# Performance work log

Hardware: AMD Instinct MI355X
Metric: run time of the kernel (lower is better)

The kernel has to match this reference:

```python
import jax, jax.numpy as jnp
import numpy as np

N_NODES = 100000
N_EDGES = 1200000
IN_CH = 64
HID = 16
OUT_CH = 64
EDGE_DIM = 3


def _glorot(key, shape):
    fan_in, fan_out = shape[0], shape[1]
    lim = float(np.sqrt(6.0 / (fan_in + fan_out)))
    return jax.random.uniform(key, shape, jnp.float32, -lim, lim)


def setup_inputs() -> dict:
    key = jax.random.key(0)
    ks = jax.random.split(key, 16)
    x = jax.random.normal(ks[0], (N_NODES, IN_CH), jnp.float32)
    edge_index = jax.random.randint(ks[1], (2, N_EDGES), 0, N_NODES, jnp.int64)
    edge_attr = jax.random.normal(ks[2], (N_EDGES, EDGE_DIM), jnp.float32)
    return {
        "x": x,
        "edge_index": edge_index,
        "edge_attr": edge_attr,
        # conv1: in->16
        "W1l": _glorot(ks[3], (IN_CH, HID)), "b1l": jnp.zeros((HID,), jnp.float32),
        "W1r": _glorot(ks[4], (IN_CH, HID)), "b1r": jnp.zeros((HID,), jnp.float32),
        "W1e": _glorot(ks[5], (EDGE_DIM, IN_CH)), "b1e": jnp.zeros((IN_CH,), jnp.float32),
        # conv2: 16->out
        "W2l": _glorot(ks[6], (HID, OUT_CH)), "b2l": jnp.zeros((OUT_CH,), jnp.float32),
        "W2r": _glorot(ks[7], (HID, OUT_CH)), "b2r": jnp.zeros((OUT_CH,), jnp.float32),
        "W2e": _glorot(ks[8], (EDGE_DIM, HID)), "b2e": jnp.zeros((HID,), jnp.float32),
    }


def _sage_conv(x, src, dst, edge_attr, We, be, Wl, bl, Wr, br):
    # message: neighbor feature + projected edge attribute (edge_dim-aware SAGE)
    msg = x[src] + edge_attr @ We + be                       # [E, C_in]
    agg = jax.ops.segment_sum(msg, dst, num_segments=N_NODES)  # [N, C_in]
    deg = jax.ops.segment_sum(jnp.ones((msg.shape[0],), msg.dtype), dst,
                              num_segments=N_NODES)
    agg = agg / jnp.maximum(deg, 1.0)[:, None]               # mean aggregation
    return agg @ Wl + bl + x @ Wr + br                       # neighbor + self paths


def reference(x, edge_index, edge_attr,
              W1l, b1l, W1r, b1r, W1e, b1e,
              W2l, b2l, W2r, b2r, W2e, b2e):
    src, dst = edge_index[0], edge_index[1]
    h = jax.nn.relu(_sage_conv(x, src, dst, edge_attr, W1e, b1e, W1l, b1l, W1r, b1r))
    # F.dropout(training=self.training): eval mode -> identity
    out = _sage_conv(h, src, dst, edge_attr, W2e, b2e, W2l, b2l, W2r, b2r)
    return out
```

## Files before the change

kernel.cpp:

```cpp
#include <hip/hip_runtime.h>
#include <hip/hip_bf16.h>
#include <stdint.h>

#define N_NODES 100000
#define N_EDGES 1200000
#define IN_CH 64
#define HID 16
#define OUT_CH 64

#define BN 100
#define NB 1000
#define BCAP 2048
#define CAP 2048

#define F_TPB 512
#define KY_BLOCKS ((N_NODES * 2 + F_TPB - 1) / F_TPB)
#define SC_EPB 2048
#define SC_EPT (SC_EPB / F_TPB)
#define SC_BLOCKS ((N_EDGES + SC_EPB - 1) / SC_EPB)
#define F_GROUPS 196

typedef __hip_bfloat16 bf16;

__device__ __forceinline__ float b2f(bf16 v) { return __bfloat162float(v); }
__device__ __forceinline__ float lo_f(uint32_t p) { return __uint_as_float(p << 16); }
__device__ __forceinline__ float hi_f(uint32_t p) { return __uint_as_float(p & 0xffff0000u); }
__device__ __forceinline__ uint16_t f2bb(float v) {
    bf16 h = __float2bfloat16(v);
    return *reinterpret_cast<uint16_t*>(&h);
}

__device__ __forceinline__ float loadf(const void* p, size_t i, int bf) {
    return bf ? b2f(((const bf16*)p)[i]) : ((const float*)p)[i];
}
__device__ __forceinline__ uint32_t bfbits(const void* p, size_t i, int bf) {
    if (bf) return ((const uint16_t*)p)[i];
    return f2bb(((const float*)p)[i]);
}
__device__ __forceinline__ int ld_dst(const int* p, int j, int i64) {
    if (i64) return ((const int2*)p)[(size_t)N_EDGES + j].x;
    return p[(size_t)N_EDGES + j];
}
__device__ __forceinline__ int ld_src(const int* p, int j, int i64) {
    if (i64) return ((const int2*)p)[j].x;
    return p[j];
}

__device__ __forceinline__ int detect_bf(const void* x) {
    const uint16_t* u = (const uint16_t*)x;
    int cnt = 0;
    for (int i = 0; i < 64; ++i) {
        int e = (u[i] >> 7) & 0xff;
        cnt += (e >= 100 && e <= 140);
    }
    return cnt >= 50;
}
__device__ __forceinline__ int detect_i64(const int* ei) {
    const uint32_t* w = (const uint32_t*)ei;
    int z = 0;
    for (int i = 1; i < 64; i += 2) z += (w[i] == 0u);
    return z >= 16;
}

__global__ void __launch_bounds__(F_TPB) k_fused(const void* __restrict__ x,
                                                 const int* __restrict__ ei,
                                                 const void* __restrict__ ea,
                                                 const void* __restrict__ W1l,
                                                 const void* __restrict__ W1r,
                                                 const void* __restrict__ b1l,
                                                 const void* __restrict__ b1r,
                                                 const void* __restrict__ W1e,
                                                 const void* __restrict__ b1e,
                                                 bf16* __restrict__ y,
                                                 bf16* __restrict__ zh,
                                                 float* __restrict__ wc,
                                                 int* __restrict__ gcnt,
                                                 uint2* __restrict__ slots,
                                                 uint16_t* __restrict__ ea2v) {
    __shared__ __align__(16) char smem[36608];
    __shared__ int wsum[8];
    __shared__ int s_flags;
    int t = threadIdx.x;
    int g = blockIdx.x / 5, r = blockIdx.x % 5;
    if (t == 0) s_flags = detect_bf(x) | (detect_i64(ei) << 1);

    if (r < 2) {
        int kyid = g * 2 + r;
        if (kyid >= KY_BLOCKS) return;
        float* w = (float*)smem;
        float* bz = (float*)(smem + 8192);
        __syncthreads();
        int bf = s_flags & 1;
        for (int i = t; i < IN_CH * 32; i += F_TPB) {
            int k = i >> 5, cc = i & 31;
            w[i] = (cc < 16) ? loadf(W1l, k * HID + cc, bf)
                             : loadf(W1r, k * HID + (cc - 16), bf);
        }
        if (t < HID) bz[t] = loadf(b1l, t, bf) + loadf(b1r, t, bf);
        __syncthreads();
        if (kyid == 0 && t < HID) {
            int j = t;
            float s0 = 0.f, s1 = 0.f, s2 = 0.f, s3 = 0.f;
            for (int k = 0; k < IN_CH; ++k) {
                float wl = w[k * 32 + j];
                s0 += loadf(W1e, k, bf) * wl;
                s1 += loadf(W1e, IN_CH + k, bf) * wl;
                s2 += loadf(W1e, 2 * IN_CH + k, bf) * wl;
                s3 += loadf(b1e, k, bf) * wl;
            }
            wc[j] = s0;
            wc[HID + j] = s1;
            wc[2 * HID + j] = s2;
            wc[3 * HID + j] = s3;
        }
        int tid = kyid * F_TPB + t;
        int row = tid >> 1;
        if (row >= N_NODES) return;
        int half = tid & 1, cs = half * 16;
        float acc[16];
#pragma unroll
        for (int j = 0; j < 16; ++j) acc[j] = 0.f;
        if (bf) {
            const uint4* xr = (const uint4*)((const uint16_t*)x + (size_t)row * IN_CH);
            uint4 q[8];
#pragma unroll
            for (int i = 0; i < 8; ++i) q[i] = xr[i];
            const uint32_t* qq = (const uint32_t*)q;
#pragma unroll
            for (int k2 = 0; k2 < 32; ++k2) {
                uint32_t u = qq[k2];
                float x0 = lo_f(u), x1 = hi_f(u);
                const float* w0 = &w[(2 * k2) * 32 + cs];
                const float* w1 = w0 + 32;
#pragma unroll
                for (int j = 0; j < 16; ++j) acc[j] += x0 * w0[j] + x1 * w1[j];
            }
        } else {
            const float4* xr = (const float4*)((const float*)x + (size_t)row * IN_CH);
#pragma unroll
            for (int c = 0; c < 4; ++c) {
                float4 f[4];
#pragma unroll
                for (int i = 0; i < 4; ++i) f[i] = xr[c * 4 + i];
                const float* ff = (const float*)f;
#pragma unroll
                for (int kk = 0; kk < 16; ++kk) {
                    float xk = ff[kk];
                    const float* wr = &w[(c * 16 + kk) * 32 + cs];
#pragma unroll
                    for (int j = 0; j < 16; ++j) acc[j] += xk * wr[j];
                }
            }
        }
        if (half) {
#pragma unroll
            for (int j = 0; j < 16; ++j) acc[j] += bz[j];
        }
        uint32_t pk[8];
#pragma unroll
        for (int j2 = 0; j2 < 8; ++j2)
            pk[j2] = (uint32_t)f2bb(acc[2 * j2]) | ((uint32_t)f2bb(acc[2 * j2 + 1]) << 16);
        bf16* dst = half ? (zh + (size_t)row * HID) : (y + (size_t)row * HID);
        uint4* d4 = (uint4*)dst;
        d4[0] = make_uint4(pk[0], pk[1], pk[2], pk[3]);
        d4[1] = make_uint4(pk[4], pk[5], pk[6], pk[7]);
        return;
    }

    int scid = g * 3 + (r - 2);
    if (scid >= SC_BLOCKS) return;
    uint2* lval = (uint2*)smem;
    int* lhist = (int*)(smem + 16384);
    int* lscan = (int*)(smem + 20384);
    int* ldelta = (int*)(smem + 24384);
    uint16_t* lea = (uint16_t*)(smem + 28384);
    uint16_t* lbid = (uint16_t*)(smem + 32480);
    for (int i = t; i < NB; i += F_TPB) lhist[i] = 0;
    __syncthreads();
    int bf = s_flags & 1, i64 = (s_flags >> 1) & 1;
    int base = scid * SC_EPB;
    uint32_t rb[SC_EPT], srcv[SC_EPT], ea01v[SC_EPT], ea2r[SC_EPT];
#pragma unroll
    for (int i = 0; i < SC_EPT; ++i) {
        int e = base + i * F_TPB + t;
        rb[i] = 0xFFFFFFFFu;
        if (e < N_EDGES) {
            uint32_t d = (uint32_t)ld_dst(ei, e, i64);
            srcv[i] = (uint32_t)ld_src(ei, e, i64);
            ea01v[i] = bfbits(ea, (size_t)e * 3, bf) |
                       (bfbits(ea, (size_t)e * 3 + 1, bf) << 16);
            ea2r[i] = bfbits(ea, (size_t)e * 3 + 2, bf);
            uint32_t b = d / BN;
            uint32_t dl = d - b * BN;
            uint32_t rr = (uint32_t)atomicAdd(&lhist[b], 1);
            rb[i] = (b << 19) | (dl << 12) | rr;
        }
    }
    __syncthreads();
    int b0 = 2 * t, b1 = 2 * t + 1;
    int cnt0 = (b0 < NB) ? lhist[b0] : 0;
    int cnt1 = (b1 < NB) ? lhist[b1] : 0;
    int s_local = cnt0 + cnt1;
    int incl = s_local;
    int lane = t & 63;
#pragma unroll
    for (int d = 1; d < 64; d <<= 1) {
        int v = __shfl_up(incl, d);
        if (lane >= d) incl += v;
    }
    int w = t >> 6;
    if (lane == 63) wsum[w] = incl;
    __syncthreads();
    int wbase = 0, nst = 0;
#pragma unroll
    for (int i = 0; i < 8; ++i) {
        int v = wsum[i];
        wbase += (i < w) ? v : 0;
        nst += v;
    }
    int run = wbase + incl - s_local;
    if (b0 < NB) {
        lscan[b0] = run;
        if (cnt0) ldelta[b0] = b0 * BCAP + atomicAdd(&gcnt[b0], cnt0) - run;
    }
    run += cnt0;
    if (b1 < NB) {
        lscan[b1] = run;
        if (cnt1) ldelta[b1] = b1 * BCAP + atomicAdd(&gcnt[b1], cnt1) - run;
    }
    __syncthreads();
#pragma unroll
    for (int i = 0; i < SC_EPT; ++i) {
        if (rb[i] == 0xFFFFFFFFu) continue;
        uint32_t b = rb[i] >> 19;
        uint32_t dl = (rb[i] >> 12) & 0x7Fu;
        uint32_t rr = rb[i] & 0xFFFu;
        int lp = lscan[b] + (int)rr;
        lval[lp] = make_uint2(srcv[i] | (dl << 17), ea01v[i]);
        lea[lp] = (uint16_t)ea2r[i];
        lbid[lp] = (uint16_t)b;
    }
    __syncthreads();
    for (int p = t; p < nst; p += F_TPB) {
        int b = lbid[p];
        int gp = ldelta[b] + p;
        slots[gp] = lval[p];
        ea2v[gp] = lea[p];
    }
}

__global__ void __launch_bounds__(256) k_agg1(const uint2* __restrict__ slots,
                                              const uint16_t* __restrict__ ea2v,
                                              const int* __restrict__ gcnt,
                                              const bf16* __restrict__ y,
                                              const float* __restrict__ wc,
                                              bf16* __restrict__ zh,
                                              float* __restrict__ sa,
                                              uint32_t* __restrict__ ssrc,
                                              int* __restrict__ nof2) {
    __shared__ uint2 su[CAP];
    __shared__ uint16_t ea2s[CAP];
    __shared__ uint32_t sst[CAP];
    __shared__ uint32_t sea01[CAP];
    __shared__ uint16_t sea2[CAP];
    __shared__ int hist[BN], noff[BN], cur[BN];
    __shared__ int wsum[4];
    __shared__ float swc[64];
    int t = threadIdx.x;
    if (t < 64) swc[t] = wc[t];
    int b = blockIdx.x;
    int n = gcnt[b];
    if (n > CAP) n = CAP;
    const uint2* sp = slots + (size_t)b * BCAP;
    const uint16_t* ep = ea2v + (size_t)b * BCAP;
    int dl = t >> 1, half = t & 1, cs = half * 8;

    for (int i = t; i < BN; i += 256) hist[i] = 0;
    for (int i = t; i < n; i += 256) {
        su[i] = sp[i];
        ea2s[i] = ep[i];
    }
    __syncthreads();
    for (int i = t; i < n; i += 256) atomicAdd(&hist[su[i].x >> 17], 1);
    __syncthreads();
    {
        int own = (t < BN) ? hist[t] : 0;
        int incl = own;
        int lane = t & 63;
#pragma unroll
        for (int d = 1; d < 64; d <<= 1) {
            int v = __shfl_up(incl, d);
            if (lane >= d) incl += v;
        }
        int w = t >> 6;
        if (lane == 63) wsum[w] = incl;
        __syncthreads();
        int wbase = 0;
#pragma unroll
        for (int i = 0; i < 4; ++i) wbase += (i < w) ? wsum[i] : 0;
        if (t < BN) {
            int ex = wbase + incl - own;
            noff[t] = ex;
            cur[t] = ex;
        }
        __syncthreads();
    }
    for (int i = t; i < n; i += 256) {
        uint2 u2 = su[i];
        int r = atomicAdd(&cur[u2.x >> 17], 1);
        sst[r] = u2.x;
        sea01[r] = u2.y;
        sea2[r] = ea2s[i];
    }
    __syncthreads();
    for (int p = t; p < n; p += 256) ssrc[(size_t)b * BCAP + p] = sst[p];
    if (t < BN) nof2[b * 128 + t] = noff[t];
    float acc[16];
#pragma unroll
    for (int j = 0; j < 16; ++j) acc[j] = 0.f;
    float a0 = 0.f, a1 = 0.f, a2 = 0.f, degT = 0.f;
    if (dl < BN) {
        int kb = noff[dl];
        int ke = (dl == BN - 1) ? n : noff[dl + 1];
        degT = (float)(ke - kb);
        int k = kb + half;
        for (; k + 2 < ke; k += 4) {
            uint32_t s0 = sst[k], s1 = sst[k + 2];
            const uint32_t* r0 = (const uint32_t*)(y + (size_t)(s0 & 0x1FFFFu) * HID);
            const uint32_t* r1 = (const uint32_t*)(y + (size_t)(s1 & 0x1FFFFu) * HID);
            uint4 qa = *(const uint4*)r0;
            uint4 qb = *(const uint4*)(r0 + 4);
            uint4 qc = *(const uint4*)r1;
            uint4 qd = *(const uint4*)(r1 + 4);
            acc[0] += lo_f(qa.x) + lo_f(qc.x); acc[1] += hi_f(qa.x) + hi_f(qc.x);
            acc[2] += lo_f(qa.y) + lo_f(qc.y); acc[3] += hi_f(qa.y) + hi_f(qc.y);
            acc[4] += lo_f(qa.z) + lo_f(qc.z); acc[5] += hi_f(qa.z) + hi_f(qc.z);
            acc[6] += lo_f(qa.w) + lo_f(qc.w); acc[7] += hi_f(qa.w) + hi_f(qc.w);
            acc[8] += lo_f(qb.x) + lo_f(qd.x); acc[9] += hi_f(qb.x) + hi_f(qd.x);
            acc[10] += lo_f(qb.y) + lo_f(qd.y); acc[11] += hi_f(qb.y) + hi_f(qd.y);
            acc[12] += lo_f(qb.z) + lo_f(qd.z); acc[13] += hi_f(qb.z) + hi_f(qd.z);
            acc[14] += lo_f(qb.w) + lo_f(qd.w); acc[15] += hi_f(qb.w) + hi_f(qd.w);
            uint32_t e0 = sea01[k], e1 = sea01[k + 2];
            a0 += lo_f(e0) + lo_f(e1);
            a1 += hi_f(e0) + hi_f(e1);
            a2 += __uint_as_float((uint32_t)sea2[k] << 16) +
                  __uint_as_float((uint32_t)sea2[k + 2] << 16);
        }
        for (; k < ke; k += 2) {
            uint32_t s0 = sst[k];
            const uint32_t* r0 = (const uint32_t*)(y + (size_t)(s0 & 0x1FFFFu) * HID);
            uint4 qa = *(const uint4*)r0;
            uint4 qb = *(const uint4*)(r0 + 4);
            acc[0] += lo_f(qa.x); acc[1] += hi_f(qa.x);
            acc[2] += lo_f(qa.y); acc[3] += hi_f(qa.y);
            acc[4] += lo_f(qa.z); acc[5] += hi_f(qa.z);
            acc[6] += lo_f(qa.w); acc[7] += hi_f(qa.w);
            acc[8] += lo_f(qb.x); acc[9] += hi_f(qb.x);
            acc[10] += lo_f(qb.y); acc[11] += hi_f(qb.y);
            acc[12] += lo_f(qb.z); acc[13] += hi_f(qb.z);
            acc[14] += lo_f(qb.w); acc[15] += hi_f(qb.w);
            uint32_t e0 = sea01[k];
            a0 += lo_f(e0);
            a1 += hi_f(e0);
            a2 += __uint_as_float((uint32_t)sea2[k] << 16);
        }
    }
    if (dl < BN) {
#pragma unroll
        for (int j = 0; j < 16; ++j) acc[j] += __shfl_xor(acc[j], 1);
        a0 += __shfl_xor(a0, 1);
        a1 += __shfl_xor(a1, 1);
        a2 += __shfl_xor(a2, 1);
        size_t i = (size_t)b * BN + dl;
        float inv = 1.0f / fmaxf(degT, 1.0f);
        uint4 zq = *(const uint4*)(zh + i * HID + cs);
        float zf[8] = {lo_f(zq.x), hi_f(zq.x), lo_f(zq.y), hi_f(zq.y),
                       lo_f(zq.z), hi_f(zq.z), lo_f(zq.w), hi_f(zq.w)};
        uint32_t pk[4];
#pragma unroll
        for (int j = 0; j < 4; ++j) {
            float t0 = (acc[cs + 2 * j] + a0 * swc[cs + 2 * j] + a1 * swc[16 + cs + 2 * j] +
                        a2 * swc[32 + cs + 2 * j] + degT * swc[48 + cs + 2 * j]) * inv;
            float t1 = (acc[cs + 2 * j + 1] + a0 * swc[cs + 2 * j + 1] + a1 * swc[17 + cs + 2 * j] +
                        a2 * swc[33 + cs + 2 * j] + degT * swc[49 + cs + 2 * j]) * inv;
            float h0 = fmaxf(t0 + zf[2 * j], 0.f);
            float h1 = fmaxf(t1 + zf[2 * j + 1], 0.f);
            pk[j] = (uint32_t)f2bb(h0) | ((uint32_t)f2bb(h1) << 16);
        }
        *(uint4*)(zh + i * HID + cs) = make_uint4(pk[0], pk[1], pk[2], pk[3]);
        if (half == 0) {
            sa[i * 3 + 0] = a0;
            sa[i * 3 + 1] = a1;
            sa[i * 3 + 2] = a2;
        }
    }
}

__global__ void __launch_bounds__(256) k_agg2(const void* __restrict__ x,
                                              const uint32_t* __restrict__ ssrc,
                                              const int* __restrict__ nof2,
                                              const int* __restrict__ gcnt,
                                              const bf16* __restrict__ zh,
                                              const float* __restrict__ sa,
                                              const void* __restrict__ W2l,
                                              const void* __restrict__ b2l,
                                              const void* __restrict__ W2r,
                                              const void* __restrict__ b2r,
                                              const void* __restrict__ W2e,
                                              const void* __restrict__ b2e,
                                              void* __restrict__ out) {
    __shared__ uint32_t ss[CAP];
    __shared__ int snoff[BN];
    __shared__ float facc[BN * HID];
    __shared__ bf16 hl[BN * HID];
    __shared__ float w2l[HID * OUT_CH];
    __shared__ float w2r[HID * OUT_CH];
    __shared__ float swe[3 * HID];
    __shared__ float sbe[HID];
    __shared__ float sbb[OUT_CH];
    __shared__ int s_bf;
    int t = threadIdx.x;
    if (t == 0) s_bf = detect_bf(x);
    __syncthreads();
    int bf = s_bf;
    for (int i = t; i < HID * OUT_CH; i += 256) {
        w2l[i] = loadf(W2l, i, bf);
        w2r[i] = loadf(W2r, i, bf);
    }
    if (t < 3 * HID) swe[t] = loadf(W2e, t, bf);
    if (t < HID) sbe[t] = loadf(b2e, t, bf);
    if (t < OUT_CH) sbb[t] = loadf(b2l, t, bf) + loadf(b2r, t, bf);
    int b = blockIdx.x;
    int n = gcnt[b];
    if (n > CAP) n = CAP;
    for (int i = t; i < n; i += 256) ss[i] = ssrc[(size_t)b * BCAP + i];
    if (t < BN) snoff[t] = nof2[b * 128 + t];
    __syncthreads();
    int dl = t >> 1, half = t & 1, cs = half * 8;
    float acc[16];
#pragma unroll
    for (int j = 0; j < 16; ++j) acc[j] = 0.f;
    float degT = 0.f;
    if (dl < BN) {
        int kb = snoff[dl];
        int ke = (dl == BN - 1) ? n : snoff[dl + 1];
        degT = (float)(ke - kb);
        int k = kb + half;
        for (; k + 2 < ke; k += 4) {
            uint32_t s0 = ss[k], s1 = ss[k + 2];
            const uint32_t* r0 = (const uint32_t*)(zh + (size_t)(s0 & 0x1FFFFu) * HID);
            const uint32_t* r1 = (const uint32_t*)(zh + (size_t)(s1 & 0x1FFFFu) * HID);
            uint4 qa = *(const uint4*)r0;
            uint4 qb = *(const uint4*)(r0 + 4);
            uint4 qc = *(const uint4*)r1;
            uint4 qd = *(const uint4*)(r1 + 4);
            acc[0] += lo_f(qa.x) + lo_f(qc.x); acc[1] += hi_f(qa.x) + hi_f(qc.x);
            acc[2] += lo_f(qa.y) + lo_f(qc.y); acc[3] += hi_f(qa.y) + hi_f(qc.y);
            acc[4] += lo_f(qa.z) + lo_f(qc.z); acc[5] += hi_f(qa.z) + hi_f(qc.z);
            acc[6] += lo_f(qa.w) + lo_f(qc.w); acc[7] += hi_f(qa.w) + hi_f(qc.w);
            acc[8] += lo_f(qb.x) + lo_f(qd.x); acc[9] += hi_f(qb.x) + hi_f(qd.x);
            acc[10] += lo_f(qb.y) + lo_f(qd.y); acc[11] += hi_f(qb.y) + hi_f(qd.y);
            acc[12] += lo_f(qb.z) + lo_f(qd.z); acc[13] += hi_f(qb.z) + hi_f(qd.z);
            acc[14] += lo_f(qb.w) + lo_f(qd.w); acc[15] += hi_f(qb.w) + hi_f(qd.w);
        }
        for (; k < ke; k += 2) {
            uint32_t s0 = ss[k];
            const uint32_t* r0 = (const uint32_t*)(zh + (size_t)(s0 & 0x1FFFFu) * HID);
            uint4 qa = *(const uint4*)r0;
            uint4 qb = *(const uint4*)(r0 + 4);
            acc[0] += lo_f(qa.x); acc[1] += hi_f(qa.x);
            acc[2] += lo_f(qa.y); acc[3] += hi_f(qa.y);
            acc[4] += lo_f(qa.z); acc[5] += hi_f(qa.z);
            acc[6] += lo_f(qa.w); acc[7] += hi_f(qa.w);
            acc[8] += lo_f(qb.x); acc[9] += hi_f(qb.x);
            acc[10] += lo_f(qb.y); acc[11] += hi_f(qb.y);
            acc[12] += lo_f(qb.z); acc[13] += hi_f(qb.z);
            acc[14] += lo_f(qb.w); acc[15] += hi_f(qb.w);
        }
    }
    if (dl < BN) {
#pragma unroll
        for (int j = 0; j < 16; ++j) acc[j] += __shfl_xor(acc[j], 1);
        size_t i = (size_t)b * BN + dl;
        float inv = 1.0f / fmaxf(degT, 1.0f);
        float a0 = sa[i * 3 + 0], a1 = sa[i * 3 + 1], a2 = sa[i * 3 + 2];
        float4 f0, f1;
        float* fo = (float*)&f0;
        float* f1o = (float*)&f1;
#pragma unroll
        for (int j = 0; j < 4; ++j) {
            fo[j] = (acc[cs + j] + a0 * swe[cs + j] + a1 * swe[16 + cs + j] +
                     a2 * swe[32 + cs + j] + degT * sbe[cs + j]) * inv;
            f1o[j] = (acc[cs + 4 + j] + a0 * swe[cs + 4 + j] + a1 * swe[16 + cs + 4 + j] +
                      a2 * swe[32 + cs + 4 + j] + degT * sbe[cs + 4 + j]) * inv;
        }
        *(float4*)&facc[dl * HID + cs] = f0;
        *(float4*)&facc[dl * HID + cs + 4] = f1;
        *(uint4*)&hl[dl * HID + cs] = *(const uint4*)(zh + i * HID + cs);
    }
    __syncthreads();
    for (int idx = t; idx < BN * OUT_CH; idx += 256) {
        int dli = idx >> 6, j = idx & 63;
        size_t i = (size_t)b * BN + dli;
        float o = sbb[j];
#pragma unroll
        for (int cc = 0; cc < HID; ++cc)
            o += facc[dli * HID + cc] * w2l[cc * OUT_CH + j] +
                 b2f(hl[dli * HID + cc]) * w2r[cc * OUT_CH + j];
        if (bf)
            ((bf16*)out)[i * OUT_CH + j] = __float2bfloat16(o);
        else
            ((float*)out)[i * OUT_CH + j] = o;
    }
}

extern "C" void kernel_launch(void* const* d_in, const int* in_sizes, int n_in,
                              void* d_out, int out_size, void* d_ws, size_t ws_size,
                              hipStream_t stream) {
    const void* x   = d_in[0];
    const int*  ei  = (const int*)d_in[1];
    const void* ea  = d_in[2];
    const void* W1l = d_in[3];
    const void* b1l = d_in[4];
    const void* W1r = d_in[5];
    const void* b1r = d_in[6];
    const void* W1e = d_in[7];
    const void* b1e = d_in[8];
    const void* W2l = d_in[9];
    const void* b2l = d_in[10];
    const void* W2r = d_in[11];
    const void* b2r = d_in[12];
    const void* W2e = d_in[13];
    const void* b2e = d_in[14];

    const size_t N16 = (size_t)N_NODES * HID;
    char* p = (char*)d_ws;
    uint2*    slots = (uint2*)p;    p += (size_t)NB * BCAP * sizeof(uint2);
    uint16_t* ea2v  = (uint16_t*)p; p += (size_t)NB * BCAP * sizeof(uint16_t);
    uint32_t* ssrc  = (uint32_t*)p; p += (size_t)NB * BCAP * sizeof(uint32_t);
    int*      nof2  = (int*)p;      p += (size_t)NB * 128 * sizeof(int);
    bf16*     y     = (bf16*)p;     p += N16 * sizeof(bf16);
    bf16*     zh    = (bf16*)p;     p += N16 * sizeof(bf16);
    float*    sa    = (float*)p;    p += (size_t)3 * N_NODES * sizeof(float);
    int*      gcnt  = (int*)p;      p += NB * sizeof(int);
    float*    wc    = (float*)p;    p += 64 * sizeof(float);

    hipMemsetAsync(gcnt, 0, NB * sizeof(int), stream);
    k_fused<<<F_GROUPS * 5, F_TPB, 0, stream>>>(x, ei, ea, W1l, W1r, b1l, b1r, W1e, b1e,
                                                y, zh, wc, gcnt, slots, ea2v);
    k_agg1<<<NB, 256, 0, stream>>>(slots, ea2v, gcnt, y, wc, zh, sa, ssrc, nof2);
    k_agg2<<<NB, 256, 0, stream>>>(x, ssrc, nof2, gcnt, zh, sa, W2l, b2l, W2r, b2r,
                                   W2e, b2e, d_out);
}
```

Baseline: 202.3 us.

## Double per-block work in fused projection/scatter kernel and halve grid size

Each projection block now computes 512 rows in two passes instead of 256. Each scatter block now bins 4096 edges instead of 2048, and the block count is halved. Because the shared staging buffer still holds only 2048 entries, the local-sort write-out runs in two passes. The launch bounds gain a min-blocks hint. The aim is to cut per-block overhead (weight staging, histogram setup, global atomics on bucket counters), at the cost of fewer blocks, more registers per thread and extra synchronisation.

```diff
diff --git a/kernel.cpp b/kernel.cpp
--- a/kernel.cpp
+++ b/kernel.cpp
@@ -14,11 +14,12 @@
 #define CAP 2048
 
 #define F_TPB 512
-#define KY_BLOCKS ((N_NODES * 2 + F_TPB - 1) / F_TPB)
-#define SC_EPB 2048
+#define KY_BLOCKS 196
+#define KY_RPB 512
+#define SC_EPB 4096
 #define SC_EPT (SC_EPB / F_TPB)
 #define SC_BLOCKS ((N_EDGES + SC_EPB - 1) / SC_EPB)
-#define F_GROUPS 196
+#define F_GROUPS 98
 
 typedef __hip_bfloat16 bf16;
 
@@ -62,21 +63,21 @@
     return z >= 16;
 }
 
-__global__ void __launch_bounds__(F_TPB) k_fused(const void* __restrict__ x,
-                                                 const int* __restrict__ ei,
-                                                 const void* __restrict__ ea,
-                                                 const void* __restrict__ W1l,
-                                                 const void* __restrict__ W1r,
-                                                 const void* __restrict__ b1l,
-                                                 const void* __restrict__ b1r,
-                                                 const void* __restrict__ W1e,
-                                                 const void* __restrict__ b1e,
-                                                 bf16* __restrict__ y,
-                                                 bf16* __restrict__ zh,
-                                                 float* __restrict__ wc,
-                                                 int* __restrict__ gcnt,
-                                                 uint2* __restrict__ slots,
-                                                 uint16_t* __restrict__ ea2v) {
+__global__ void __launch_bounds__(F_TPB, 4) k_fused(const void* __restrict__ x,
+                                                    const int* __restrict__ ei,
+                                                    const void* __restrict__ ea,
+                                                    const void* __restrict__ W1l,
+                                                    const void* __restrict__ W1r,
+                                                    const void* __restrict__ b1l,
+                                                    const void* __restrict__ b1r,
+                                                    const void* __restrict__ W1e,
+                                                    const void* __restrict__ b1e,
+                                                    bf16* __restrict__ y,
+                                                    bf16* __restrict__ zh,
+                                                    float* __restrict__ wc,
+                                                    int* __restrict__ gcnt,
+                                                    uint2* __restrict__ slots,
+                                                    uint16_t* __restrict__ ea2v) {
     __shared__ __align__(16) char smem[36608];
     __shared__ int wsum[8];
     __shared__ int s_flags;
@@ -86,7 +87,6 @@
 
     if (r < 2) {
         int kyid = g * 2 + r;
-        if (kyid >= KY_BLOCKS) return;
         float* w = (float*)smem;
         float* bz = (float*)(smem + 8192);
         __syncthreads();
@@ -113,57 +113,58 @@
             wc[2 * HID + j] = s2;
             wc[3 * HID + j] = s3;
         }
-        int tid = kyid * F_TPB + t;
-        int row = tid >> 1;
-        if (row >= N_NODES) return;
-        int half = tid & 1, cs = half * 16;
-        float acc[16];
-#pragma unroll
-        for (int j = 0; j < 16; ++j) acc[j] = 0.f;
-        if (bf) {
-            const uint4* xr = (const uint4*)((const uint16_t*)x + (size_t)row * IN_CH);
-            uint4 q[8];
-#pragma unroll
-            for (int i = 0; i < 8; ++i) q[i] = xr[i];
-            const uint32_t* qq = (const uint32_t*)q;
-#pragma unroll
-            for (int k2 = 0; k2 < 32; ++k2) {
-                uint32_t u = qq[k2];
-                float x0 = lo_f(u), x1 = hi_f(u);
-                const float* w0 = &w[(2 * k2) * 32 + cs];
-                const float* w1 = w0 + 32;
-#pragma unroll
-                for (int j = 0; j < 16; ++j) acc[j] += x0 * w0[j] + x1 * w1[j];
-            }
-        } else {
-            const float4* xr = (const float4*)((const float*)x + (size_t)row * IN_CH);
-#pragma unroll
-            for (int c = 0; c < 4; ++c) {
-                float4 f[4];
-#pragma unroll
-                for (int i = 0; i < 4; ++i) f[i] = xr[c * 4 + i];
-                const float* ff = (const float*)f;
-#pragma unroll
-                for (int kk = 0; kk < 16; ++kk) {
-                    float xk = ff[kk];
-                    const float* wr = &w[(c * 16 + kk) * 32 + cs];
-#pragma unroll
-                    for (int j = 0; j < 16; ++j) acc[j] += xk * wr[j];
+        int half = t & 1, cs = half * 16;
+        for (int rep = 0; rep < 2; ++rep) {
+            int row = kyid * KY_RPB + rep * 256 + (t >> 1);
+            if (row >= N_NODES) continue;
+            float acc[16];
+#pragma unroll
+            for (int j = 0; j < 16; ++j) acc[j] = 0.f;
+            if (bf) {
+                const uint4* xr = (const uint4*)((const uint16_t*)x + (size_t)row * IN_CH);
+                uint4 q[8];
+#pragma unroll
+                for (int i = 0; i < 8; ++i) q[i] = xr[i];
+                const uint32_t* qq = (const uint32_t*)q;
+#pragma unroll
+                for (int k2 = 0; k2 < 32; ++k2) {
+                    uint32_t u = qq[k2];
+                    float x0 = lo_f(u), x1 = hi_f(u);
+                    const float* w0 = &w[(2 * k2) * 32 + cs];
+                    const float* w1 = w0 + 32;
+#pragma unroll
+                    for (int j = 0; j < 16; ++j) acc[j] += x0 * w0[j] + x1 * w1[j];
+                }
+            } else {
+                const float4* xr = (const float4*)((const float*)x + (size_t)row * IN_CH);
+#pragma unroll
+                for (int c = 0; c < 4; ++c) {
+                    float4 f[4];
+#pragma unroll
+                    for (int i = 0; i < 4; ++i) f[i] = xr[c * 4 + i];
+                    const float* ff = (const float*)f;
+#pragma unroll
+                    for (int kk = 0; kk < 16; ++kk) {
+                        float xk = ff[kk];
+                        const float* wr = &w[(c * 16 + kk) * 32 + cs];
+#pragma unroll
+                        for (int j = 0; j < 16; ++j) acc[j] += xk * wr[j];
+                    }
                 }
             }
-        }
-        if (half) {
-#pragma unroll
-            for (int j = 0; j < 16; ++j) acc[j] += bz[j];
-        }
-        uint32_t pk[8];
-#pragma unroll
-        for (int j2 = 0; j2 < 8; ++j2)
-            pk[j2] = (uint32_t)f2bb(acc[2 * j2]) | ((uint32_t)f2bb(acc[2 * j2 + 1]) << 16);
-        bf16* dst = half ? (zh + (size_t)row * HID) : (y + (size_t)row * HID);
-        uint4* d4 = (uint4*)dst;
-        d4[0] = make_uint4(pk[0], pk[1], pk[2], pk[3]);
-        d4[1] = make_uint4(pk[4], pk[5], pk[6], pk[7]);
+            if (half) {
+#pragma unroll
+                for (int j = 0; j < 16; ++j) acc[j] += bz[j];
+            }
+            uint32_t pk[8];
+#pragma unroll
+            for (int j2 = 0; j2 < 8; ++j2)
+                pk[j2] = (uint32_t)f2bb(acc[2 * j2]) | ((uint32_t)f2bb(acc[2 * j2 + 1]) << 16);
+            bf16* dst = half ? (zh + (size_t)row * HID) : (y + (size_t)row * HID);
+            uint4* d4 = (uint4*)dst;
+            d4[0] = make_uint4(pk[0], pk[1], pk[2], pk[3]);
+            d4[1] = make_uint4(pk[4], pk[5], pk[6], pk[7]);
+        }
         return;
     }
 
@@ -236,16 +237,43 @@
         uint32_t dl = (rb[i] >> 12) & 0x7Fu;
         uint32_t rr = rb[i] & 0xFFFu;
         int lp = lscan[b] + (int)rr;
-        lval[lp] = make_uint2(srcv[i] | (dl << 17), ea01v[i]);
-        lea[lp] = (uint16_t)ea2r[i];
-        lbid[lp] = (uint16_t)b;
-    }
-    __syncthreads();
-    for (int p = t; p < nst; p += F_TPB) {
+        if (lp < 2048) {
+            lval[lp] = make_uint2(srcv[i] | (dl << 17), ea01v[i]);
+            lea[lp] = (uint16_t)ea2r[i];
+            lbid[lp] = (uint16_t)b;
+        }
+    }
+    __syncthreads();
+    int lim = nst < 2048 ? nst : 2048;
+    for (int p = t; p < lim; p += F_TPB) {
         int b = lbid[p];
         int gp = ldelta[b] + p;
         slots[gp] = lval[p];
         ea2v[gp] = lea[p];
+    }
+    if (nst > 2048) {
+        __syncthreads();
+#pragma unroll
+        for (int i = 0; i < SC_EPT; ++i) {
+            if (rb[i] == 0xFFFFFFFFu) continue;
+            uint32_t b = rb[i] >> 19;
+            uint32_t dl = (rb[i] >> 12) & 0x7Fu;
+            uint32_t rr = rb[i] & 0xFFFu;
+            int lp = lscan[b] + (int)rr - 2048;
+            if (lp >= 0) {
+                lval[lp] = make_uint2(srcv[i] | (dl << 17), ea01v[i]);
+                lea[lp] = (uint16_t)ea2r[i];
+                lbid[lp] = (uint16_t)b;
+            }
+        }
+        __syncthreads();
+        int n2 = nst - 2048;
+        for (int p2 = t; p2 < n2; p2 += F_TPB) {
+            int b = lbid[p2];
+            int gp = ldelta[b] + p2 + 2048;
+            slots[gp] = lval[p2];
+            ea2v[gp] = lea[p2];
+        }
     }
 }
 
```

After: 198.1 us. 2.0% less time.
